# Kernel tuning notes

Hardware: AMD Instinct MI355X
Metric: run time of the kernel (lower is better)

Reference implementation:

```python
import jax, jax.numpy as jnp
import numpy as np

B, L = 16, 2048          # batch, raw history length
H, S, M = 512, 8, 512    # hidden_dim, sequence_count, max_seq_len
V = 32000                # shared embed_tokens vocab
TG = 64                  # TIME_GAP_BUCKET_COUNT
LN_EPS = 1e-5


def setup_inputs() -> dict:
    key = jax.random.key(0)
    ks = jax.random.split(key, 16)
    f = lambda k, shp, scale=0.02: jax.random.normal(k, shp, jnp.float32) * scale
    return {
        "history_tokens": jax.random.randint(ks[0], (B, L), 0, V),
        "history_post_tokens": jax.random.randint(ks[1], (B, L), 0, V),
        "history_author_tokens": jax.random.randint(ks[2], (B, L), 0, V),
        "history_action_tokens": jax.random.randint(ks[3], (B, L), 0, V),
        "history_time_gap": jax.random.randint(ks[4], (B, L), 0, TG + 1),
        "history_group_ids": jax.random.randint(ks[5], (B, L), 0, S + 1),
        "history_mask": jax.random.randint(ks[6], (B, L), 0, 2).astype(bool),
        "embed_table": f(ks[7], (V, H)),
        "time_gap_table": f(ks[8], (TG + 1, H)).at[0].set(0.0),   # padding_idx=0
        "seq_id_table": f(ks[9], (S + 1, H)).at[0].set(0.0),      # padding_idx=0
        "pos_table": f(ks[10], (M, H)),
        "ln_gamma": jnp.ones((5 * H,), jnp.float32),
        "ln_beta": jnp.zeros((5 * H,), jnp.float32),
        "w1": f(ks[11], (5 * H, 4 * H)),
        "b1": jnp.zeros((4 * H,), jnp.float32),
        "w2": f(ks[12], (4 * H, H)),
        "b2": jnp.zeros((H,), jnp.float32),
        "empty_tokens": f(ks[13], (S, H)),
    }


def _forward(embed_table, time_gap_table, seq_id_table, pos_table, ln_gamma, ln_beta,
             w1, b1, w2, b2, empty_tokens,
             history_tokens, history_post_tokens, history_author_tokens,
             history_action_tokens, history_time_gap, history_group_ids, history_mask):
    # --- event feature construction: 4 shared-vocab lookups + time-gap embedding ---
    h = embed_table[history_tokens]            # [B,L,H]
    p = embed_table[history_post_tokens]
    a = embed_table[history_author_tokens]
    act = embed_table[history_action_tokens]
    gap_idx = jnp.clip(history_time_gap, 0, TG)
    gap = time_gap_table[gap_idx] * (gap_idx != 0)[..., None]  # padding_idx=0 -> zero vec
    x = jnp.concatenate([h, p, a, act, gap], axis=-1)           # [B,L,5H]

    # --- event_projection: LayerNorm -> Linear -> SiLU -> (Dropout eval) -> Linear ---
    mu = x.mean(-1, keepdims=True)
    var = x.var(-1, keepdims=True)
    xn = (x - mu) * jax.lax.rsqrt(var + LN_EPS) * ln_gamma + ln_beta
    mid = jax.nn.silu(xn @ w1 + b1)                             # [B,L,4H]
    event = mid @ w2 + b2                                       # [B,L,H]

    # --- ragged regroup: for each (b, s) gather masked positions with group id s+1,
    #     keep the LAST M of them, scatter to slots 0..count-1 ---
    gid = history_group_ids                                     # [B,L]
    match = history_mask[:, None, :] & (gid[:, None, :] == jnp.arange(1, S + 1)[None, :, None])  # [B,S,L]
    cum = jnp.cumsum(match.astype(jnp.int32), axis=-1)          # rank+1 within group
    count = cum[..., -1]                                        # [B,S]
    offset = jnp.maximum(count - M, 0)                          # drop all but last M
    slot = cum - 1 - offset[..., None]                          # [B,S,L]
    keep = match & (slot >= 0)
    slot = jnp.where(keep, slot, M)                             # M is out-of-range -> dropped

    b_idx = jnp.arange(B)[:, None, None]
    s_idx = jnp.arange(S)[None, :, None]
    states = jnp.zeros((B, S, M, H), event.dtype)
    states = states.at[b_idx, s_idx, slot].set(event[:, None, :, :], mode="drop")
    smask = jnp.zeros((B, S, M), bool)
    smask = smask.at[b_idx, s_idx, slot].set(True, mode="drop")

    # empty groups get the learned empty token at slot 0
    empty = count == 0                                          # [B,S]
    states = states.at[:, :, 0, :].set(
        jnp.where(empty[..., None], empty_tokens[None], states[:, :, 0, :]))
    smask = smask.at[:, :, 0].set(smask[:, :, 0] | empty)

    # positional + sequence-id embeddings, then zero padded slots
    pos = pos_table[None, None]                                 # [1,1,M,H]
    sid = seq_id_table[1:S + 1][None, :, None, :]               # [1,S,1,H]
    states = (states + pos + sid) * smask[..., None].astype(states.dtype)
    return states, smask


def reference(history_tokens, history_post_tokens, history_author_tokens,
              history_action_tokens, history_time_gap, history_group_ids, history_mask,
              embed_table, time_gap_table, seq_id_table, pos_table, ln_gamma, ln_beta,
              w1, b1, w2, b2, empty_tokens):
    return _forward(embed_table, time_gap_table, seq_id_table, pos_table, ln_gamma, ln_beta,
                    w1, b1, w2, b2, empty_tokens,
                    history_tokens, history_post_tokens, history_author_tokens,
                    history_action_tokens, history_time_gap, history_group_ids, history_mask)
```

## Files before the change

kernel.cpp:

```cpp
#include <hip/hip_runtime.h>
#include <hip/hip_bf16.h>
#include <stdint.h>

#define B_ 16
#define L_ 2048
#define H_ 512
#define S_ 8
#define M_ 512
#define TG_ 64
#define NTOK (B_ * L_)
#define FIVEH (5 * H_)
#define FOURH (4 * H_)

typedef __attribute__((ext_vector_type(4))) float f32x4;
typedef __attribute__((ext_vector_type(8))) short bf16x8;

__device__ __forceinline__ short f2bf(float f) {
  unsigned u = __builtin_bit_cast(unsigned, f);
  unsigned r = (u + 0x7FFFu + ((u >> 16) & 1u)) >> 16;
  return (short)r;
}

__device__ __forceinline__ void gload_lds16(const void* g, void* l) {
  __builtin_amdgcn_global_load_lds(
      (const __attribute__((address_space(1))) unsigned int*)g,
      (__attribute__((address_space(3))) unsigned int*)l, 16, 0, 0);
}

#define BAR __builtin_amdgcn_s_barrier()
#define LGKM0 do { asm volatile("s_waitcnt lgkmcnt(0)" ::: "memory"); \
                   __builtin_amdgcn_sched_barrier(0); } while (0)
#define VMW(n) asm volatile("s_waitcnt vmcnt(" #n ")" ::: "memory")
#define PRIO(p) __builtin_amdgcn_s_setprio(p)


#define STAGE(src, isB, slot, half, kt) do {                                  \
    const short* _s = (src) + (size_t)((half) * 128) * K + (kt);              \
    const int _o = ((isB) ? 65536 : 0) + (slot) * 32768 + (half) * 16384;     \
    gload_lds16(_s + (size_t)sr0 * K + sc0, lds + _o + db0);                  \
    gload_lds16(_s + (size_t)sr1 * K + sc1, lds + _o + db1);                  \
  } while (0)

#define LDA(qr, slot) do { const int _b = (slot) * 32768 + aW + (qr) * 8192;  \
    _Pragma("unroll") for (int fm = 0; fm < 4; ++fm)                          \
    _Pragma("unroll") for (int ks = 0; ks < 2; ++ks)                          \
      a[fm][ks] = *(const bf16x8*)(lds + _b + sA[fm][ks]); } while (0)

#define LDB(dst, qc, slot) do { const int _b = (slot) * 32768 + bW + (qc) * 4096; \
    _Pragma("unroll") for (int fn = 0; fn < 2; ++fn)                          \
    _Pragma("unroll") for (int ks = 0; ks < 2; ++ks)                          \
      dst[fn][ks] = *(const bf16x8*)(lds + _b + sB[fn][ks]); } while (0)

#define MFMA16(qr, qc, bs) do {                                               \
    _Pragma("unroll") for (int fm = 0; fm < 4; ++fm)                          \
    _Pragma("unroll") for (int fn = 0; fn < 2; ++fn)                          \
    _Pragma("unroll") for (int ks = 0; ks < 2; ++ks)                          \
      acc[(qr)*4+fm][(qc)*2+fn] = __builtin_amdgcn_mfma_f32_16x16x32_bf16(    \
          a[fm][ks], bs[fn][ks], acc[(qr)*4+fm][(qc)*2+fn], 0, 0, 0); } while (0)

template<int K>
__device__ __forceinline__ void gemm_core(const short* __restrict__ Ag,
                                          const short* __restrict__ Bg,
                                          char* lds, f32x4 (&acc)[8][4],
                                          int tid) {
  constexpr int NITER = K / 128;
  const int lane = tid & 63;
  const int wave = tid >> 6;
  const int wm = wave >> 2;
  const int wn = wave & 3;
  const int la = lane & 15;
  const int hi = lane >> 4;

  const int x = (la & 7) << 4;
  int sA[4][2], sB[2][2];
#pragma unroll
  for (int fm = 0; fm < 4; ++fm)
#pragma unroll
    for (int ks = 0; ks < 2; ++ks)
      sA[fm][ks] = (((fm * 16 + la) * 128) + (ks * 32 + hi * 8) * 2) ^ x;
#pragma unroll
  for (int fn = 0; fn < 2; ++fn)
#pragma unroll
    for (int ks = 0; ks < 2; ++ks)
      sB[fn][ks] = ((((wn & 1) * 64 + fn * 16 + la) * 128) + (ks * 32 + hi * 8) * 2) ^ x;
  const int aW = wm * 16384;
  const int bW = 65536 + (wn >> 1) * 16384;

  const int db0 = tid * 16, db1 = tid * 16 + 8192;
  const int lb0 = db0 ^ (((db0 >> 7) & 7) << 4);
  const int lb1 = db1 ^ (((db1 >> 7) & 7) << 4);
  const int sr0 = lb0 >> 7, sc0 = (lb0 & 127) >> 1;
  const int sr1 = lb1 >> 7, sc1 = (lb1 & 127) >> 1;

  bf16x8 a[4][2], b0v[2][2], b1v[2][2];

  STAGE(Bg, 1, 0, 0, 0); STAGE(Bg, 1, 0, 1, 0);
  STAGE(Ag, 0, 0, 0, 0); STAGE(Ag, 0, 0, 1, 0);
  STAGE(Bg, 1, 1, 0, 64); STAGE(Bg, 1, 1, 1, 64);
  VMW(0);
  BAR;

  for (int i = 0; i < NITER - 1; ++i) {
    const int kt1 = (2 * i + 1) * 64, kt2 = kt1 + 64, kt3 = kt1 + 128;
    LDA(0, 0); LDB(b0v, 0, 0); STAGE(Ag, 0, 1, 0, kt1);
    BAR; LGKM0; PRIO(1); MFMA16(0, 0, b0v); PRIO(0); BAR;
    LDB(b1v, 1, 0); STAGE(Ag, 0, 1, 1, kt1);
    BAR; LGKM0; PRIO(1); MFMA16(0, 1, b1v); PRIO(0); BAR;
    LDA(1, 0); STAGE(Bg, 1, 0, 0, kt2);
    BAR; LGKM0; PRIO(1); MFMA16(1, 1, b1v); PRIO(0); BAR;
    STAGE(Bg, 1, 0, 1, kt2);
    BAR; LGKM0; PRIO(1); MFMA16(1, 0, b0v); PRIO(0); VMW(4); BAR;
    LDA(0, 1); LDB(b0v, 0, 1); STAGE(Ag, 0, 0, 0, kt2);
    BAR; LGKM0; PRIO(1); MFMA16(0, 0, b0v); PRIO(0); BAR;
    LDB(b1v, 1, 1); STAGE(Ag, 0, 0, 1, kt2);
    BAR; LGKM0; PRIO(1); MFMA16(0, 1, b1v); PRIO(0); BAR;
    LDA(1, 1); STAGE(Bg, 1, 1, 0, kt3);
    BAR; LGKM0; PRIO(1); MFMA16(1, 1, b1v); PRIO(0); BAR;
    STAGE(Bg, 1, 1, 1, kt3);
    BAR; LGKM0; PRIO(1); MFMA16(1, 0, b0v); PRIO(0); VMW(4); BAR;
  }
  {
    const int kt1 = (2 * (NITER - 1) + 1) * 64;
    LDA(0, 0); LDB(b0v, 0, 0); STAGE(Ag, 0, 1, 0, kt1);
    BAR; LGKM0; PRIO(1); MFMA16(0, 0, b0v); PRIO(0); BAR;
    LDB(b1v, 1, 0); STAGE(Ag, 0, 1, 1, kt1);
    BAR; LGKM0; PRIO(1); MFMA16(0, 1, b1v); PRIO(0); BAR;
    LDA(1, 0);
    BAR; LGKM0; PRIO(1); MFMA16(1, 1, b1v); PRIO(0); BAR;
    BAR; LGKM0; PRIO(1); MFMA16(1, 0, b0v); PRIO(0); VMW(0); BAR;
    LDA(0, 1); LDB(b0v, 0, 1);
    BAR; LGKM0; PRIO(1); MFMA16(0, 0, b0v); PRIO(0); BAR;
    LDB(b1v, 1, 1);
    BAR; LGKM0; PRIO(1); MFMA16(0, 1, b1v); PRIO(0); BAR;
    LDA(1, 1);
    BAR; LGKM0; PRIO(1); MFMA16(1, 1, b1v); PRIO(0); BAR;
    BAR; LGKM0; PRIO(1); MFMA16(1, 0, b0v); PRIO(0);
  }
}

__global__ __launch_bounds__(512, 2) void gemm1_kernel(
    const short* __restrict__ A, const short* __restrict__ Bt,
    const float* __restrict__ bias, const int* __restrict__ nkeep,
    short* __restrict__ C) {
  const int bn = blockIdx.x & 7;
  const int bm = blockIdx.x >> 3;
  if (bm * 256 >= nkeep[0]) return;
  __shared__ __align__(16) char lds[131072];
  const int tid = threadIdx.x;
  f32x4 acc[8][4] = {};
  gemm_core<FIVEH>(A + (size_t)bm * 256 * FIVEH, Bt + (size_t)bn * 256 * FIVEH,
                   lds, acc, tid);
  const int lane = tid & 63, wave = tid >> 6;
  const int wm = wave >> 2, wn = wave & 3;
  const int la = lane & 15, hi = lane >> 4;
  const int row0 = bm * 256 + wm * 128 + hi * 4;
  const int col0 = bn * 256 + wn * 64 + la;
#pragma unroll
  for (int mi = 0; mi < 8; ++mi)
#pragma unroll
    for (int ni = 0; ni < 4; ++ni) {
      const int col = col0 + ni * 16;
      const float bv = bias[col];
#pragma unroll
      for (int r = 0; r < 4; ++r) {
        const int row = row0 + mi * 16 + r;
        float v = acc[mi][ni][r] + bv;
        float sg = 1.f / (1.f + __expf(-v));
        C[(size_t)row * FOURH + col] = f2bf(v * sg);
      }
    }
}

#define ASL(s) ((s) * 32768)
#define BSL(s) (98304 + (s) * 16384)

#define STG2(src, ldsoff, kt) do {                                            \
    const short* _s = (src) + (kt);                                          \
    gload_lds16(_s + (size_t)sr0 * 2048 + sc0, lds + (ldsoff) + db0);         \
    gload_lds16(_s + (size_t)sr1 * 2048 + sc1, lds + (ldsoff) + db1);         \
  } while (0)

#define LDA2(slot) do { const int _b = ASL(slot) + aW2;                       \
    _Pragma("unroll") for (int fm = 0; fm < 4; ++fm)                          \
    _Pragma("unroll") for (int ks = 0; ks < 2; ++ks)                          \
      a[fm][ks] = *(const bf16x8*)(lds + _b + sA2[fm][ks]); } while (0)

#define LDB2a(slot) do { const int _b = BSL(slot);                            \
    _Pragma("unroll") for (int fn = 0; fn < 2; ++fn)                          \
    _Pragma("unroll") for (int ks = 0; ks < 2; ++ks)                          \
      b[fn][ks] = *(const bf16x8*)(lds + _b + sB2[fn][ks]); } while (0)

#define LDB2b(slot) do { const int _b = BSL(slot);                            \
    _Pragma("unroll") for (int fn = 2; fn < 4; ++fn)                          \
    _Pragma("unroll") for (int ks = 0; ks < 2; ++ks)                          \
      b[fn][ks] = *(const bf16x8*)(lds + _b + sB2[fn][ks]); } while (0)

#define MFMA2(h) do {                                                         \
    _Pragma("unroll") for (int fm = 0; fm < 4; ++fm)                          \
    _Pragma("unroll") for (int fn = 2*(h); fn < 2*(h)+2; ++fn)                \
    _Pragma("unroll") for (int ks = 0; ks < 2; ++ks)                          \
      acc[fm][fn] = __builtin_amdgcn_mfma_f32_16x16x32_bf16(                  \
          a[fm][ks], b[fn][ks], acc[fm][fn], 0, 0, 0); } while (0)

#define T2(slot, kt, ISSUE, WAITC) do {                                       \
    LDA2(slot); LDB2a(slot);                                                  \
    if (ISSUE) STG2(Ag, ASL(((slot) + 2) % 3), kt);                           \
    BAR; LGKM0; PRIO(1); MFMA2(0); PRIO(0); BAR;                              \
    LDB2b(slot);                                                              \
    if (ISSUE) { STG2(Ag + 128 * 2048, ASL(((slot) + 2) % 3) + 16384, kt);    \
                 STG2(Bg, BSL(((slot) + 2) % 3), kt); }                       \
    BAR; LGKM0; PRIO(1); MFMA2(1); PRIO(0); WAITC; BAR;                       \
  } while (0)

__global__ __launch_bounds__(512) void gemm2_kernel(
    const short* __restrict__ A, const short* __restrict__ Bt,
    const float* __restrict__ b2, const float* __restrict__ pos,
    const float* __restrict__ sidtab, const int* __restrict__ destv,
    const int* __restrict__ nkeep, float* __restrict__ states) {
  const int bn = blockIdx.x & 3;
  const int bm = blockIdx.x >> 2;
  const int nk = nkeep[0];
  if (bm * 256 >= nk) return;
  __shared__ __align__(16) char lds[147456];
  const int tid = threadIdx.x;
  const int lane = tid & 63, wave = tid >> 6;
  const int wm = wave >> 1;
  const int wn = wave & 1;
  const int la = lane & 15, hi = lane >> 4;
  const short* Ag = A + (size_t)bm * 256 * 2048;
  const short* Bg = Bt + (size_t)bn * 128 * 2048;

  const int x = (la & 7) << 4;
  int sA2[4][2], sB2[4][2];
#pragma unroll
  for (int fm = 0; fm < 4; ++fm)
#pragma unroll
    for (int ks = 0; ks < 2; ++ks)
      sA2[fm][ks] = ((((wm & 1) * 64 + fm * 16 + la) * 128) + (ks * 32 + hi * 8) * 2) ^ x;
#pragma unroll
  for (int fn = 0; fn < 4; ++fn)
#pragma unroll
    for (int ks = 0; ks < 2; ++ks)
      sB2[fn][ks] = (((wn * 64 + fn * 16 + la) * 128) + (ks * 32 + hi * 8) * 2) ^ x;
  const int aW2 = (wm >> 1) * 16384;

  const int db0 = tid * 16, db1 = tid * 16 + 8192;
  const int lb0 = db0 ^ (((db0 >> 7) & 7) << 4);
  const int lb1 = db1 ^ (((db1 >> 7) & 7) << 4);
  const int sr0 = lb0 >> 7, sc0 = (lb0 & 127) >> 1;
  const int sr1 = lb1 >> 7, sc1 = (lb1 & 127) >> 1;

  f32x4 acc[4][4] = {};
  bf16x8 a[4][2], b[4][2];

  STG2(Ag, ASL(0), 0); STG2(Ag + 128 * 2048, ASL(0) + 16384, 0); STG2(Bg, BSL(0), 0);
  STG2(Ag, ASL(1), 64); STG2(Ag + 128 * 2048, ASL(1) + 16384, 64); STG2(Bg, BSL(1), 64);
  VMW(6);
  BAR;
  for (int i = 0; i < 10; ++i) {
    const int kt = i * 192 + 128;
    T2(0, kt, true, VMW(6));
    T2(1, kt + 64, true, VMW(6));
    T2(2, kt + 128, true, VMW(6));
  }
  T2(0, 0, false, VMW(0));
  T2(1, 0, false, ((void)0));

  const int row0 = bm * 256 + wm * 64 + hi * 4;
  const int col0 = bn * 128 + wn * 64 + la;
#pragma unroll
  for (int mi = 0; mi < 4; ++mi) {
#pragma unroll
    for (int r = 0; r < 4; ++r) {
      const int row = row0 + mi * 16 + r;
      if (row >= nk) continue;
      const int dest = destv[row];
      const int slot = dest & (M_ - 1);
      const int gs = dest >> 9;
      const int s = gs & (S_ - 1);
      float* orow = states + (size_t)dest * H_;
#pragma unroll
      for (int n = 0; n < 4; ++n) {
        const int col = col0 + n * 16;
        orow[col] = acc[mi][n][r] + b2[col] + pos[slot * H_ + col] +
                    sidtab[(s + 1) * H_ + col];
      }
    }
  }
}

__global__ __launch_bounds__(256) void transpose_cvt_kernel(
    const float* __restrict__ in, short* __restrict__ out, int K, int N) {
  __shared__ float tile[32][33];
  const int n0 = blockIdx.x * 32, k0 = blockIdx.y * 32;
  const int tx = threadIdx.x, ty = threadIdx.y;
#pragma unroll
  for (int i = 0; i < 32; i += 8)
    tile[ty + i][tx] = in[(size_t)(k0 + ty + i) * N + n0 + tx];
  __syncthreads();
#pragma unroll
  for (int i = 0; i < 32; i += 8)
    out[(size_t)(n0 + ty + i) * K + k0 + tx] = f2bf(tile[tx][ty + i]);
}

__global__ __launch_bounds__(256) void scan_kernel(
    const int* __restrict__ gid, const int* __restrict__ mask,
    int* __restrict__ rankv, int* __restrict__ counts) {
  const int b = blockIdx.x >> 3;
  const int s = blockIdx.x & 7;
  const int g = s + 1;
  const int base = b * L_;
  const int t = threadIdx.x;
  int loc = 0, sum = 0;
  const int l0 = t * 8;
#pragma unroll
  for (int j = 0; j < 8; ++j) {
    int l = l0 + j;
    bool mt = (mask[base + l] != 0) && (gid[base + l] == g);
    loc |= (mt ? 1 : 0) << j;
    sum += mt ? 1 : 0;
  }
  __shared__ int lds[256];
  lds[t] = sum;
  __syncthreads();
  for (int off = 1; off < 256; off <<= 1) {
    int vv = (t >= off) ? lds[t - off] : 0;
    __syncthreads();
    lds[t] += vv;
    __syncthreads();
  }
  int run = lds[t] - sum;
#pragma unroll
  for (int j = 0; j < 8; ++j) {
    if ((loc >> j) & 1) {
      run += 1;
      rankv[base + l0 + j] = run;
    }
  }
  if (t == 0) counts[blockIdx.x] = lds[255];
}

__global__ __launch_bounds__(256) void compact_kernel(
    const int* __restrict__ rankv, const int* __restrict__ counts,
    const int* __restrict__ gid, int* __restrict__ tokidx,
    int* __restrict__ destv, int* __restrict__ nkeep) {
  const int token = blockIdx.x * 256 + threadIdx.x;
  const int t = threadIdx.x;
  const int r = rankv[token];
  int dest = -1;
  if (r > 0) {
    const int g = gid[token];
    const int b = token >> 11;
    const int gs = b * S_ + (g - 1);
    const int cnt = counts[gs];
    const int over = cnt - M_;
    const int slot = r - 1 - (over > 0 ? over : 0);
    if (slot >= 0) dest = gs * M_ + slot;
  }
  const int flag = (dest >= 0) ? 1 : 0;
  __shared__ int lds[256];
  __shared__ int basep;
  lds[t] = flag;
  __syncthreads();
  for (int off = 1; off < 256; off <<= 1) {
    int vv = (t >= off) ? lds[t - off] : 0;
    __syncthreads();
    lds[t] += vv;
    __syncthreads();
  }
  if (t == 255) basep = atomicAdd(nkeep, lds[255]);
  __syncthreads();
  if (flag) {
    const int p = basep + lds[t] - 1;
    tokidx[p] = token;
    destv[p] = dest;
  }
}

__global__ __launch_bounds__(256) void gather_ln_kernel(
    const int* __restrict__ tokidx, const int* __restrict__ nkeep,
    const int* __restrict__ tok0, const int* __restrict__ tok1,
    const int* __restrict__ tok2, const int* __restrict__ tok3,
    const int* __restrict__ tgap,
    const float* __restrict__ emb, const float* __restrict__ gaptab,
    const float* __restrict__ gamma, const float* __restrict__ beta,
    short* __restrict__ xn) {
  const int wid = threadIdx.x >> 6;
  const int l = threadIdx.x & 63;
  const int j = blockIdx.x * 4 + wid;
  const int nk = nkeep[0];
  const int padded = (nk + 255) & ~255;
  if (j >= padded) return;
  short* orow = xn + (size_t)j * FIVEH;
  if (j >= nk) {
    short4 z = make_short4(0, 0, 0, 0);
#pragma unroll
    for (int i = 0; i < 10; ++i) ((short4*)orow)[i * 64 + l] = z;
    return;
  }
  const int token = tokidx[j];
  const int tk0 = tok0[token], tk1 = tok1[token], tk2 = tok2[token],
            tk3 = tok3[token];
  int gi = tgap[token];
  gi = gi < 0 ? 0 : (gi > TG_ ? TG_ : gi);
  const float4* sb[5];
  sb[0] = (const float4*)(emb + (size_t)tk0 * H_);
  sb[1] = (const float4*)(emb + (size_t)tk1 * H_);
  sb[2] = (const float4*)(emb + (size_t)tk2 * H_);
  sb[3] = (const float4*)(emb + (size_t)tk3 * H_);
  sb[4] = (const float4*)(gaptab + (size_t)gi * H_);
  float4 v[10];
  float sum = 0.f, sq = 0.f;
#pragma unroll
  for (int i = 0; i < 10; ++i) {
    const int d4 = i * 64 + l;
    const int seg = i >> 1;
    float4 xv;
    if (seg < 4 || gi != 0) xv = sb[seg][d4 & 127];
    else xv = make_float4(0.f, 0.f, 0.f, 0.f);
    v[i] = xv;
    sum += xv.x + xv.y + xv.z + xv.w;
    sq += xv.x * xv.x + xv.y * xv.y + xv.z * xv.z + xv.w * xv.w;
  }
#pragma unroll
  for (int s = 32; s; s >>= 1) {
    sum += __shfl_xor(sum, s, 64);
    sq += __shfl_xor(sq, s, 64);
  }
  const float mu = sum * (1.f / FIVEH);
  const float var = sq * (1.f / FIVEH) - mu * mu;
  const float rs = rsqrtf(var + 1e-5f);
#pragma unroll
  for (int i = 0; i < 10; ++i) {
    const int d4 = i * 64 + l;
    const float4 g4 = ((const float4*)gamma)[d4];
    const float4 b4 = ((const float4*)beta)[d4];
    short4 o;
    o.x = f2bf((v[i].x - mu) * rs * g4.x + b4.x);
    o.y = f2bf((v[i].y - mu) * rs * g4.y + b4.y);
    o.z = f2bf((v[i].z - mu) * rs * g4.z + b4.z);
    o.w = f2bf((v[i].w - mu) * rs * g4.w + b4.w);
    ((short4*)orow)[d4] = o;
  }
}

__global__ __launch_bounds__(256) void finalize_kernel(
    const int* __restrict__ counts, const float* __restrict__ empty_tok,
    const float* __restrict__ pos, const float* __restrict__ sidtab,
    float* __restrict__ states, float* __restrict__ smask) {
  const int total = B_ * S_ * M_ * (H_ / 4);
  for (int idx = blockIdx.x * 256 + threadIdx.x; idx < total;
       idx += gridDim.x * 256) {
    const int row = idx >> 7, c = idx & 127;
    const int gs = row >> 9, m = row & (M_ - 1), s = gs & (S_ - 1);
    const int cnt = counts[gs];
    const bool empty = (cnt == 0);
    const bool filled = m < (cnt < M_ ? cnt : M_);
    if (c == 0) smask[row] = (filled || (empty && m == 0)) ? 1.0f : 0.0f;
    if (filled) continue;
    float4 o = make_float4(0.f, 0.f, 0.f, 0.f);
    if (empty && m == 0) {
      float4 e = ((const float4*)(empty_tok + s * H_))[c];
      float4 pv = ((const float4*)pos)[c];
      float4 sd = ((const float4*)(sidtab + (s + 1) * H_))[c];
      o.x = e.x + pv.x + sd.x;
      o.y = e.y + pv.y + sd.y;
      o.z = e.z + pv.z + sd.z;
      o.w = e.w + pv.w + sd.w;
    }
    ((float4*)(states + (size_t)row * H_))[c] = o;
  }
}

extern "C" void kernel_launch(void* const* d_in, const int* in_sizes, int n_in,
                              void* d_out, int out_size, void* d_ws, size_t ws_size,
                              hipStream_t stream) {
  const int* tok0 = (const int*)d_in[0];
  const int* tok1 = (const int*)d_in[1];
  const int* tok2 = (const int*)d_in[2];
  const int* tok3 = (const int*)d_in[3];
  const int* tgap = (const int*)d_in[4];
  const int* gid = (const int*)d_in[5];
  const int* mask = (const int*)d_in[6];
  const float* emb = (const float*)d_in[7];
  const float* gaptab = (const float*)d_in[8];
  const float* sidtab = (const float*)d_in[9];
  const float* pos = (const float*)d_in[10];
  const float* gamma = (const float*)d_in[11];
  const float* beta = (const float*)d_in[12];
  const float* w1 = (const float*)d_in[13];
  const float* b1 = (const float*)d_in[14];
  const float* w2 = (const float*)d_in[15];
  const float* b2 = (const float*)d_in[16];
  const float* empty_tok = (const float*)d_in[17];

  char* p = (char*)d_ws;
  short* xn = (short*)p;  p += (size_t)NTOK * FIVEH * 2;
  short* mid = (short*)p; p += (size_t)NTOK * FOURH * 2;
  short* w1T = (short*)p; p += (size_t)FOURH * FIVEH * 2;
  short* w2T = (short*)p; p += (size_t)H_ * FOURH * 2;
  int* rankv = (int*)p;   p += (size_t)NTOK * 4;
  int* tokidx = (int*)p;  p += (size_t)NTOK * 4;
  int* destv = (int*)p;   p += (size_t)NTOK * 4;
  int* counts = (int*)p;  p += 512;
  int* nkeep = (int*)p;   p += 512;

  float* states = (float*)d_out;
  float* smask = states + (size_t)B_ * S_ * M_ * H_;

  hipMemsetAsync(rankv, 0, (size_t)NTOK * 4, stream);
  hipMemsetAsync(nkeep, 0, 4, stream);
  transpose_cvt_kernel<<<dim3(FOURH / 32, FIVEH / 32), dim3(32, 8), 0, stream>>>(
      w1, w1T, FIVEH, FOURH);
  transpose_cvt_kernel<<<dim3(H_ / 32, FOURH / 32), dim3(32, 8), 0, stream>>>(
      w2, w2T, FOURH, H_);
  scan_kernel<<<B_ * S_, 256, 0, stream>>>(gid, mask, rankv, counts);
  compact_kernel<<<NTOK / 256, 256, 0, stream>>>(rankv, counts, gid, tokidx,
                                                 destv, nkeep);
  gather_ln_kernel<<<NTOK / 4, 256, 0, stream>>>(tokidx, nkeep, tok0, tok1, tok2,
                                                 tok3, tgap, emb, gaptab, gamma,
                                                 beta, xn);
  gemm1_kernel<<<128 * 8, 512, 0, stream>>>(xn, w1T, b1, nkeep, mid);
  gemm2_kernel<<<128 * 4, 512, 0, stream>>>(mid, w2T, b2, pos, sidtab, destv,
                                            nkeep, states);
  finalize_kernel<<<2048, 256, 0, stream>>>(counts, empty_tok, pos, sidtab,
                                            states, smask);
}
```

Measured before the change: 277.7 us.

## Fuse scan with compaction, merge weight transposes, remap gemm1 block order

```diff
diff --git a/kernel.cpp b/kernel.cpp
--- a/kernel.cpp
+++ b/kernel.cpp
@@ -142,9 +142,11 @@
     const short* __restrict__ A, const short* __restrict__ Bt,
     const float* __restrict__ bias, const int* __restrict__ nkeep,
     short* __restrict__ C) {
-  const int bn = blockIdx.x & 7;
-  const int bm = blockIdx.x >> 3;
-  if (bm * 256 >= nkeep[0]) return;
+  const int nbm = (nkeep[0] + 255) >> 8;
+  const int local = blockIdx.x >> 3;
+  if (local >= nbm) return;
+  const int T = (blockIdx.x & 7) * nbm + local;
+  const int bm = T >> 3, bn = T & 7;
   __shared__ __align__(16) char lds[131072];
   const int tid = threadIdx.x;
   f32x4 acc[8][4] = {};
@@ -290,9 +292,16 @@
 }
 
 __global__ __launch_bounds__(256) void transpose_cvt_kernel(
-    const float* __restrict__ in, short* __restrict__ out, int K, int N) {
+    const float* __restrict__ w1, short* __restrict__ w1T,
+    const float* __restrict__ w2, short* __restrict__ w2T) {
+  const float* in;
+  short* out;
+  int K, N;
+  if (blockIdx.z == 0) { in = w1; out = w1T; K = FIVEH; N = FOURH; }
+  else                 { in = w2; out = w2T; K = FOURH; N = H_; }
+  const int n0 = blockIdx.x * 32, k0 = blockIdx.y * 32;
+  if (n0 >= N || k0 >= K) return;
   __shared__ float tile[32][33];
-  const int n0 = blockIdx.x * 32, k0 = blockIdx.y * 32;
   const int tx = threadIdx.x, ty = threadIdx.y;
 #pragma unroll
   for (int i = 0; i < 32; i += 8)
@@ -305,7 +314,8 @@
 
 __global__ __launch_bounds__(256) void scan_kernel(
     const int* __restrict__ gid, const int* __restrict__ mask,
-    int* __restrict__ rankv, int* __restrict__ counts) {
+    int* __restrict__ counts, int* __restrict__ tokidx,
+    int* __restrict__ destv, int* __restrict__ nkeep) {
   const int b = blockIdx.x >> 3;
   const int s = blockIdx.x & 7;
   const int g = s + 1;
@@ -321,6 +331,7 @@
     sum += mt ? 1 : 0;
   }
   __shared__ int lds[256];
+  __shared__ int basep, offs;
   lds[t] = sum;
   __syncthreads();
   for (int off = 1; off < 256; off <<= 1) {
@@ -329,51 +340,26 @@
     lds[t] += vv;
     __syncthreads();
   }
+  if (t == 255) {
+    const int cnt = lds[255];
+    counts[blockIdx.x] = cnt;
+    const int kc = cnt < M_ ? cnt : M_;
+    offs = cnt - kc;
+    basep = atomicAdd(nkeep, kc);
+  }
+  __syncthreads();
   int run = lds[t] - sum;
+  const int gsM = blockIdx.x * M_;
 #pragma unroll
   for (int j = 0; j < 8; ++j) {
     if ((loc >> j) & 1) {
       run += 1;
-      rankv[base + l0 + j] = run;
+      const int slot = run - 1 - offs;
+      if (slot >= 0) {
+        tokidx[basep + slot] = base + l0 + j;
+        destv[basep + slot] = gsM + slot;
+      }
     }
-  }
-  if (t == 0) counts[blockIdx.x] = lds[255];
-}
-
-__global__ __launch_bounds__(256) void compact_kernel(
-    const int* __restrict__ rankv, const int* __restrict__ counts,
-    const int* __restrict__ gid, int* __restrict__ tokidx,
-    int* __restrict__ destv, int* __restrict__ nkeep) {
-  const int token = blockIdx.x * 256 + threadIdx.x;
-  const int t = threadIdx.x;
-  const int r = rankv[token];
-  int dest = -1;
-  if (r > 0) {
-    const int g = gid[token];
-    const int b = token >> 11;
-    const int gs = b * S_ + (g - 1);
-    const int cnt = counts[gs];
-    const int over = cnt - M_;
-    const int slot = r - 1 - (over > 0 ? over : 0);
-    if (slot >= 0) dest = gs * M_ + slot;
-  }
-  const int flag = (dest >= 0) ? 1 : 0;
-  __shared__ int lds[256];
-  __shared__ int basep;
-  lds[t] = flag;
-  __syncthreads();
-  for (int off = 1; off < 256; off <<= 1) {
-    int vv = (t >= off) ? lds[t - off] : 0;
-    __syncthreads();
-    lds[t] += vv;
-    __syncthreads();
-  }
-  if (t == 255) basep = atomicAdd(nkeep, lds[255]);
-  __syncthreads();
-  if (flag) {
-    const int p = basep + lds[t] - 1;
-    tokidx[p] = token;
-    destv[p] = dest;
   }
 }
 
@@ -499,7 +485,6 @@
   short* mid = (short*)p; p += (size_t)NTOK * FOURH * 2;
   short* w1T = (short*)p; p += (size_t)FOURH * FIVEH * 2;
   short* w2T = (short*)p; p += (size_t)H_ * FOURH * 2;
-  int* rankv = (int*)p;   p += (size_t)NTOK * 4;
   int* tokidx = (int*)p;  p += (size_t)NTOK * 4;
   int* destv = (int*)p;   p += (size_t)NTOK * 4;
   int* counts = (int*)p;  p += 512;
@@ -508,15 +493,11 @@
   float* states = (float*)d_out;
   float* smask = states + (size_t)B_ * S_ * M_ * H_;
 
-  hipMemsetAsync(rankv, 0, (size_t)NTOK * 4, stream);
   hipMemsetAsync(nkeep, 0, 4, stream);
-  transpose_cvt_kernel<<<dim3(FOURH / 32, FIVEH / 32), dim3(32, 8), 0, stream>>>(
-      w1, w1T, FIVEH, FOURH);
-  transpose_cvt_kernel<<<dim3(H_ / 32, FOURH / 32), dim3(32, 8), 0, stream>>>(
-      w2, w2T, FOURH, H_);
-  scan_kernel<<<B_ * S_, 256, 0, stream>>>(gid, mask, rankv, counts);
-  compact_kernel<<<NTOK / 256, 256, 0, stream>>>(rankv, counts, gid, tokidx,
-                                                 destv, nkeep);
+  transpose_cvt_kernel<<<dim3(FOURH / 32, FIVEH / 32, 2), dim3(32, 8), 0, stream>>>(
+      w1, w1T, w2, w2T);
+  scan_kernel<<<B_ * S_, 256, 0, stream>>>(gid, mask, counts, tokidx, destv,
+                                           nkeep);
   gather_ln_kernel<<<NTOK / 4, 256, 0, stream>>>(tokidx, nkeep, tok0, tok1, tok2,
                                                  tok3, tgap, emb, gaptab, gamma,
                                                  beta, xn);
```

After: 264.6 us. 4.7% less time.
